# Kernel tuning notes

Hardware: AMD Instinct MI355X
Metric: run time of the kernel (lower is better)

Reference implementation:

```python
import jax, jax.numpy as jnp
import numpy as np

B, D_IN, D_OUT = 8192, 4096, 4096
IN_DIMS = (64, 64)
OUT_DIMS = (64, 64)
# tt_rank_rate=0.5 over dims [64,64,64,64] -> ranks [1,32,1024,32,1]
RANKS = (1, 32, 1024, 32, 1)


def _kaiming_uniform(key, shape):
    # matches nn.init.kaiming_uniform_(a=sqrt(5)) on a (r_prev, d, r) tensor:
    # fan_in = prod(shape[1:]) = d * r, gain = sqrt(2/(1+5)) = sqrt(1/3)
    fan_in = shape[1] * shape[2]
    bound = np.sqrt(1.0 / 3.0) * np.sqrt(3.0 / fan_in)
    return jax.random.uniform(key, shape, jnp.float32, -bound, bound)


def setup_inputs() -> dict:
    key = jax.random.key(0)
    kx, k0, k1, k2, k3, kb = jax.random.split(key, 6)
    dims = list(IN_DIMS) + list(OUT_DIMS)
    shapes = [(RANKS[i], dims[i], RANKS[i + 1]) for i in range(4)]
    x = jax.random.normal(kx, (B, D_IN), jnp.float32)
    core0 = _kaiming_uniform(k0, shapes[0])  # (1, 64, 32)
    core1 = _kaiming_uniform(k1, shapes[1])  # (32, 64, 1024)
    core2 = _kaiming_uniform(k2, shapes[2])  # (1024, 64, 32)
    core3 = _kaiming_uniform(k3, shapes[3])  # (32, 64, 1)
    bb = 1.0 / np.sqrt(D_IN)
    bias = jax.random.uniform(kb, (D_OUT,), jnp.float32, -bb, bb)
    return {"x": x, "core0": core0, "core1": core1, "core2": core2,
            "core3": core3, "bias": bias}


def reference(x, core0, core1, core2, core3, bias):
    b = x.shape[0]
    s = x.reshape(b, IN_DIMS[0], IN_DIMS[1])          # (B, 64, 64)
    # input core 0: contract first input dim (rank-in = 1 squeezed)
    s = jnp.einsum('bcd,cs->bds', s, core0[0])        # (B, 64, 32)
    # input core 1: contract second input dim and rank
    s = jnp.einsum('bcr,rcs->bs', s, core1)           # (B, 1024)
    # output core 2: expand first output dim
    s = jnp.einsum('br,rAs->bAs', s, core2)           # (B, 64, 32)
    # output core 3: expand second output dim (rank-out = 1 squeezed)
    s = jnp.einsum('bAr,rB->bAB', s, core3[..., 0])   # (B, 64, 64)
    return s.reshape(b, -1) + bias                    # (B, 4096)
```

## Files before the change

### kernel.cpp

```cpp
#include <hip/hip_runtime.h>
#include <hip/hip_bf16.h>


typedef _Float16 h4 __attribute__((ext_vector_type(4)));
typedef _Float16 h8 __attribute__((ext_vector_type(8)));
typedef float f32x4 __attribute__((ext_vector_type(4)));

#define BATCH 8192

__device__ __forceinline__ void gld_lds16(const void* g, void* l) {
  __builtin_amdgcn_global_load_lds(
      (__attribute__((address_space(1))) void*)(g),
      (__attribute__((address_space(3))) void*)(l), 16, 0, 0);
}

template <int PERM>
__global__ __launch_bounds__(256) void transpose_cast(
    const float* __restrict__ src, _Float16* __restrict__ dst, int K, int U) {
  __shared__ float t[64][65];
  const int k0 = blockIdx.x * 64, u0 = blockIdx.y * 64;
  const int tx = threadIdx.x & 63, ty = threadIdx.x >> 6;
  for (int i = ty; i < 64; i += 4) {
    const int k = k0 + i;
    const int sr = PERM ? ((k & 31) * 64 + (k >> 5)) : k;
    t[i][tx] = src[(size_t)sr * U + u0 + tx];
  }
  __syncthreads();
  for (int i = ty; i < 64; i += 4) {
    dst[(size_t)(u0 + i) * K + k0 + tx] = (_Float16)t[tx][i];
  }
}

__global__ __launch_bounds__(256) void stage2(const float* __restrict__ x,
                                              const float* __restrict__ c0,
                                              _Float16* __restrict__ s1) {
  __shared__ _Float16 xh[4 * 4096];
  __shared__ float c0l[2048];
  const int b0 = blockIdx.x * 4;
  const int tid = threadIdx.x;

  {
    const float4* xg = (const float4*)(x + (size_t)b0 * 4096);
#pragma unroll
    for (int k = 0; k < 16; ++k) {
      float4 v = xg[tid + 256 * k];
      h4 w = {(_Float16)v.x, (_Float16)v.y, (_Float16)v.z, (_Float16)v.w};
      ((h4*)xh)[tid + 256 * k] = w;
    }
    ((float4*)c0l)[tid] = ((const float4*)c0)[tid];
    ((float4*)c0l)[tid + 256] = ((const float4*)c0)[tid + 256];
  }
  __syncthreads();

  const int row = tid >> 6, t6 = tid & 63;
  const int d0 = (t6 >> 3) * 8;
  const int r0 = (t6 & 7) * 4;
  const _Float16* xrow = xh + row * 4096;

  float acc[8][4];
#pragma unroll
  for (int i = 0; i < 8; ++i)
#pragma unroll
    for (int j = 0; j < 4; ++j) acc[i][j] = 0.0f;

  for (int c = 0; c < 64; ++c) {
    h8 xv = *(const h8*)&xrow[c * 64 + d0];
    f32x4 wv = *(const f32x4*)&c0l[c * 32 + r0];
#pragma unroll
    for (int i = 0; i < 8; ++i) {
      const float xf = (float)xv[i];
#pragma unroll
      for (int j = 0; j < 4; ++j) acc[i][j] += xf * wv[j];
    }
  }

  _Float16* s1row = s1 + (size_t)(b0 + row) * 2048;
#pragma unroll
  for (int i = 0; i < 8; ++i) {
    h4 o = {(_Float16)acc[i][0], (_Float16)acc[i][1], (_Float16)acc[i][2],
            (_Float16)acc[i][3]};
    *(h4*)&s1row[(d0 + i) * 32 + r0] = o;
  }
}

template <int M, int N, int K>
__global__ __launch_bounds__(256, 3) void gemm_tn(
    const _Float16* __restrict__ A, const _Float16* __restrict__ Bt,
    _Float16* __restrict__ C) {
  __shared__ _Float16 lA[128 * 64];
  __shared__ _Float16 lB[128 * 64];
  const int bm = blockIdx.x, bn = blockIdx.y;
  const int tid = threadIdx.x;
  const int w = tid >> 6, lane = tid & 63;
  const int wm = (w >> 1) << 6, wn = (w & 1) << 6;
  const int lr = lane & 15, kh = lane >> 4;

  f32x4 acc[4][4] = {};

  const int sr = (w << 5) + (lane >> 3);
  const int sc = ((lane & 7) ^ (lane >> 3)) << 4;
  const char* gA = (const char*)(A + (size_t)(bm * 128 + sr) * K) + sc;
  const char* gB = (const char*)(Bt + (size_t)(bn * 128 + sr) * K) + sc;
  char* lAw = (char*)lA + w * 4096;
  char* lBw = (char*)lB + w * 4096;

  for (int kt = 0; kt < K / 64; ++kt) {
    __syncthreads();
    const size_t go = (size_t)kt * 128;
#pragma unroll
    for (int i = 0; i < 4; ++i) {
      gld_lds16(gA + go + (size_t)(i * 8) * (K * 2), lAw + i * 1024);
      gld_lds16(gB + go + (size_t)(i * 8) * (K * 2), lBw + i * 1024);
    }
    __syncthreads();
#pragma unroll
    for (int kk = 0; kk < 2; ++kk) {
      h8 af[4], bf[4];
#pragma unroll
      for (int m = 0; m < 4; ++m) {
        const int R = wm + m * 16 + lr;
        af[m] = *(const h8*)((const char*)lA + R * 128 +
                             ((((kk << 2) + kh) ^ (R & 7)) << 4));
      }
#pragma unroll
      for (int n = 0; n < 4; ++n) {
        const int R = wn + n * 16 + lr;
        bf[n] = *(const h8*)((const char*)lB + R * 128 +
                             ((((kk << 2) + kh) ^ (R & 7)) << 4));
      }
#pragma unroll
      for (int m = 0; m < 4; ++m)
#pragma unroll
        for (int n = 0; n < 4; ++n)
          acc[m][n] = __builtin_amdgcn_mfma_f32_16x16x32_f16(af[m], bf[n],
                                                             acc[m][n], 0, 0, 0);
    }
  }

#pragma unroll
  for (int m = 0; m < 4; ++m) {
    const int r0 = bm * 128 + wm + m * 16 + kh * 4;
#pragma unroll
    for (int n = 0; n < 4; ++n) {
      const int c0 = bn * 128 + wn + n * 16 + lr;
#pragma unroll
      for (int q = 0; q < 4; ++q)
        C[(size_t)(r0 + q) * N + c0] = (_Float16)acc[m][n][q];
    }
  }
}

__global__ __launch_bounds__(256) void stage5(const _Float16* __restrict__ s3,
                                              const float* __restrict__ c3,
                                              const float* __restrict__ bias,
                                              float* __restrict__ out) {
  __shared__ float s3t[4][2048];
  __shared__ float c3l[2048];
  const int b0 = blockIdx.x * 4;
  const int tid = threadIdx.x;
  const int row = tid >> 6, t6 = tid & 63;

  {
    const _Float16* sg = s3 + (size_t)(b0 + row) * 2048;
    const int Aj = t6 & 15, t0 = (t6 >> 4) * 8;
#pragma unroll
    for (int k = 0; k < 4; ++k) {
      const int A = Aj + 16 * k;
      h8 v = *(const h8*)&sg[A * 32 + t0];
#pragma unroll
      for (int u = 0; u < 8; ++u) s3t[row][(t0 + u) * 64 + A] = (float)v[u];
    }
    ((float4*)c3l)[tid] = ((const float4*)c3)[tid];
    ((float4*)c3l)[tid + 256] = ((const float4*)c3)[tid + 256];
  }
  __syncthreads();

  const int A0 = (t6 >> 3) * 8;
  const int B0 = (t6 & 7) * 8;

  float acc[8][8];
#pragma unroll
  for (int i = 0; i < 8; ++i)
#pragma unroll
    for (int j = 0; j < 8; ++j) acc[i][j] = 0.0f;

  for (int t = 0; t < 32; ++t) {
    f32x4 sa0 = *(const f32x4*)&s3t[row][t * 64 + A0];
    f32x4 sa1 = *(const f32x4*)&s3t[row][t * 64 + A0 + 4];
    f32x4 cb0 = *(const f32x4*)&c3l[t * 64 + B0];
    f32x4 cb1 = *(const f32x4*)&c3l[t * 64 + B0 + 4];
#pragma unroll
    for (int i = 0; i < 4; ++i) {
#pragma unroll
      for (int j = 0; j < 4; ++j) {
        acc[i][j] += sa0[i] * cb0[j];
        acc[i][j + 4] += sa0[i] * cb1[j];
        acc[i + 4][j] += sa1[i] * cb0[j];
        acc[i + 4][j + 4] += sa1[i] * cb1[j];
      }
    }
  }

  float* orow = out + (size_t)(b0 + row) * 4096;
#pragma unroll
  for (int i = 0; i < 8; ++i) {
    const int o = (A0 + i) * 64 + B0;
    f32x4 bv0 = *(const f32x4*)&bias[o];
    f32x4 bv1 = *(const f32x4*)&bias[o + 4];
    f32x4 r0, r1;
#pragma unroll
    for (int j = 0; j < 4; ++j) {
      r0[j] = acc[i][j] + bv0[j];
      r1[j] = acc[i][j + 4] + bv1[j];
    }
    *(f32x4*)&orow[o] = r0;
    *(f32x4*)&orow[o + 4] = r1;
  }
}

extern "C" void kernel_launch(void* const* d_in, const int* in_sizes, int n_in,
                              void* d_out, int out_size, void* d_ws,
                              size_t ws_size, hipStream_t stream) {
  (void)in_sizes; (void)n_in; (void)out_size; (void)ws_size;
  const float* x     = (const float*)d_in[0];
  const float* core0 = (const float*)d_in[1];
  const float* core1 = (const float*)d_in[2];
  const float* core2 = (const float*)d_in[3];
  const float* core3 = (const float*)d_in[4];
  const float* bias  = (const float*)d_in[5];
  float* out = (float*)d_out;

  char* ws = (char*)d_ws;
  _Float16* s1h = (_Float16*)ws;
  _Float16* s2h = (_Float16*)(ws + 33554432);
  _Float16* W1t = (_Float16*)(ws + 50331648);
  _Float16* W2t = (_Float16*)(ws + 54525952);

  transpose_cast<1><<<dim3(32, 16), 256, 0, stream>>>(core1, W1t, 2048, 1024);
  transpose_cast<0><<<dim3(16, 32), 256, 0, stream>>>(core2, W2t, 1024, 2048);
  stage2<<<BATCH / 4, 256, 0, stream>>>(x, core0, s1h);
  gemm_tn<BATCH, 1024, 2048><<<dim3(BATCH / 128, 1024 / 128), 256, 0, stream>>>(s1h, W1t, s2h);
  gemm_tn<BATCH, 2048, 1024><<<dim3(BATCH / 128, 2048 / 128), 256, 0, stream>>>(s2h, W2t, s1h);
  stage5<<<BATCH / 4, 256, 0, stream>>>(s1h, core3, bias, out);
}
```

Measured before the change: 175.7 us.

## Fuse core3 contraction and bias into second GEMM epilogue via MFMA

The second TT GEMM now stages its fp16 tile in LDS and runs the core3 contraction (rank 32 to 64 outputs) as extra MFMA ops. It then adds bias and writes fp32 output directly, which removes the stage5 kernel and the round-trip of the 32 MB intermediate through global memory. The two weight transpose kernels are also merged into one launch. In exchange, the core3 contraction now uses fp16 inputs instead of fp32, and the epilogue makes strided scattered stores to the output.

```diff
diff --git a/kernel.cpp b/kernel.cpp
--- a/kernel.cpp
+++ b/kernel.cpp
@@ -14,15 +14,20 @@
       (__attribute__((address_space(3))) void*)(l), 16, 0, 0);
 }
 
-template <int PERM>
-__global__ __launch_bounds__(256) void transpose_cast(
-    const float* __restrict__ src, _Float16* __restrict__ dst, int K, int U) {
+__global__ __launch_bounds__(256) void transpose_cast2(
+    const float* __restrict__ c1, _Float16* __restrict__ W1t,
+    const float* __restrict__ c2, _Float16* __restrict__ W2t) {
   __shared__ float t[64][65];
-  const int k0 = blockIdx.x * 64, u0 = blockIdx.y * 64;
+  const int which = blockIdx.z;
+  const float* src = which ? c2 : c1;
+  _Float16* dst = which ? W2t : W1t;
+  const int K = which ? 1024 : 2048, U = which ? 2048 : 1024;
+  const int k0 = (which ? blockIdx.y : blockIdx.x) * 64;
+  const int u0 = (which ? blockIdx.x : blockIdx.y) * 64;
   const int tx = threadIdx.x & 63, ty = threadIdx.x >> 6;
   for (int i = ty; i < 64; i += 4) {
     const int k = k0 + i;
-    const int sr = PERM ? ((k & 31) * 64 + (k >> 5)) : k;
+    const int sr = which ? k : ((k & 31) * 64 + (k >> 5));
     t[i][tx] = src[(size_t)sr * U + u0 + tx];
   }
   __syncthreads();
@@ -150,71 +155,112 @@
   }
 }
 
-__global__ __launch_bounds__(256) void stage5(const _Float16* __restrict__ s3,
-                                              const float* __restrict__ c3,
-                                              const float* __restrict__ bias,
-                                              float* __restrict__ out) {
-  __shared__ float s3t[4][2048];
-  __shared__ float c3l[2048];
-  const int b0 = blockIdx.x * 4;
+template <int M, int K>
+__global__ __launch_bounds__(256, 3) void gemm2_fused(
+    const _Float16* __restrict__ A, const _Float16* __restrict__ Bt,
+    const float* __restrict__ c3, const float* __restrict__ bias,
+    float* __restrict__ out) {
+  __shared__ _Float16 lds[128 * 128];
+  _Float16* lA = lds;
+  _Float16* lB = lds + 128 * 64;
+  const int bm = blockIdx.x, bn = blockIdx.y;
   const int tid = threadIdx.x;
-  const int row = tid >> 6, t6 = tid & 63;
-
-  {
-    const _Float16* sg = s3 + (size_t)(b0 + row) * 2048;
-    const int Aj = t6 & 15, t0 = (t6 >> 4) * 8;
-#pragma unroll
-    for (int k = 0; k < 4; ++k) {
-      const int A = Aj + 16 * k;
-      h8 v = *(const h8*)&sg[A * 32 + t0];
-#pragma unroll
-      for (int u = 0; u < 8; ++u) s3t[row][(t0 + u) * 64 + A] = (float)v[u];
-    }
-    ((float4*)c3l)[tid] = ((const float4*)c3)[tid];
-    ((float4*)c3l)[tid + 256] = ((const float4*)c3)[tid + 256];
-  }
-  __syncthreads();
-
-  const int A0 = (t6 >> 3) * 8;
-  const int B0 = (t6 & 7) * 8;
-
-  float acc[8][8];
-#pragma unroll
-  for (int i = 0; i < 8; ++i)
-#pragma unroll
-    for (int j = 0; j < 8; ++j) acc[i][j] = 0.0f;
-
-  for (int t = 0; t < 32; ++t) {
-    f32x4 sa0 = *(const f32x4*)&s3t[row][t * 64 + A0];
-    f32x4 sa1 = *(const f32x4*)&s3t[row][t * 64 + A0 + 4];
-    f32x4 cb0 = *(const f32x4*)&c3l[t * 64 + B0];
-    f32x4 cb1 = *(const f32x4*)&c3l[t * 64 + B0 + 4];
+  const int w = tid >> 6, lane = tid & 63;
+  const int wm = (w >> 1) << 6, wn = (w & 1) << 6;
+  const int lr = lane & 15, kh = lane >> 4;
+
+  f32x4 acc[4][4] = {};
+
+  const int sr = (w << 5) + (lane >> 3);
+  const int sc = ((lane & 7) ^ (lane >> 3)) << 4;
+  const char* gA = (const char*)(A + (size_t)(bm * 128 + sr) * K) + sc;
+  const char* gB = (const char*)(Bt + (size_t)(bn * 128 + sr) * K) + sc;
+  char* lAw = (char*)lA + w * 4096;
+  char* lBw = (char*)lB + w * 4096;
+
+  for (int kt = 0; kt < K / 64; ++kt) {
+    __syncthreads();
+    const size_t go = (size_t)kt * 128;
 #pragma unroll
     for (int i = 0; i < 4; ++i) {
-#pragma unroll
-      for (int j = 0; j < 4; ++j) {
-        acc[i][j] += sa0[i] * cb0[j];
-        acc[i][j + 4] += sa0[i] * cb1[j];
-        acc[i + 4][j] += sa1[i] * cb0[j];
-        acc[i + 4][j + 4] += sa1[i] * cb1[j];
-      }
-    }
-  }
-
-  float* orow = out + (size_t)(b0 + row) * 4096;
-#pragma unroll
-  for (int i = 0; i < 8; ++i) {
-    const int o = (A0 + i) * 64 + B0;
-    f32x4 bv0 = *(const f32x4*)&bias[o];
-    f32x4 bv1 = *(const f32x4*)&bias[o + 4];
-    f32x4 r0, r1;
-#pragma unroll
-    for (int j = 0; j < 4; ++j) {
-      r0[j] = acc[i][j] + bv0[j];
-      r1[j] = acc[i][j + 4] + bv1[j];
-    }
-    *(f32x4*)&orow[o] = r0;
-    *(f32x4*)&orow[o + 4] = r1;
+      gld_lds16(gA + go + (size_t)(i * 8) * (K * 2), lAw + i * 1024);
+      gld_lds16(gB + go + (size_t)(i * 8) * (K * 2), lBw + i * 1024);
+    }
+    __syncthreads();
+#pragma unroll
+    for (int kk = 0; kk < 2; ++kk) {
+      h8 af[4], bf[4];
+#pragma unroll
+      for (int m = 0; m < 4; ++m) {
+        const int R = wm + m * 16 + lr;
+        af[m] = *(const h8*)((const char*)lA + R * 128 +
+                             ((((kk << 2) + kh) ^ (R & 7)) << 4));
+      }
+#pragma unroll
+      for (int n = 0; n < 4; ++n) {
+        const int R = wn + n * 16 + lr;
+        bf[n] = *(const h8*)((const char*)lB + R * 128 +
+                             ((((kk << 2) + kh) ^ (R & 7)) << 4));
+      }
+#pragma unroll
+      for (int m = 0; m < 4; ++m)
+#pragma unroll
+        for (int n = 0; n < 4; ++n)
+          acc[m][n] = __builtin_amdgcn_mfma_f32_16x16x32_f16(af[m], bf[n],
+                                                             acc[m][n], 0, 0, 0);
+    }
+  }
+
+  __syncthreads();
+
+  h8 bfe[4];
+  float bb[4][4];
+#pragma unroll
+  for (int n = 0; n < 4; ++n) {
+#pragma unroll
+    for (int j = 0; j < 8; ++j)
+      bfe[n][j] = (_Float16)c3[(kh * 8 + j) * 64 + n * 16 + lr];
+#pragma unroll
+    for (int a = 0; a < 4; ++a)
+      bb[a][n] = bias[bn * 256 + a * 64 + n * 16 + lr];
+  }
+
+#pragma unroll
+  for (int m = 0; m < 4; ++m) {
+    const int Rb = wm + m * 16 + kh * 4;
+#pragma unroll
+    for (int n = 0; n < 4; ++n) {
+      const int cc = wn + n * 16 + lr;
+#pragma unroll
+      for (int q = 0; q < 4; ++q) {
+        const int R = Rb + q;
+        const int byte =
+            R * 256 + ((((cc >> 3) ^ (R & 7)) << 4) | ((cc & 7) << 1));
+        *(_Float16*)((char*)lds + byte) = (_Float16)acc[m][n][q];
+      }
+    }
+  }
+  __syncthreads();
+
+  const int wrow = w << 5;
+#pragma unroll
+  for (int mi = 0; mi < 2; ++mi) {
+    const int row = wrow + mi * 16 + lr;
+    const int orow0 = bm * 128 + wrow + mi * 16 + kh * 4;
+#pragma unroll
+    for (int a = 0; a < 4; ++a) {
+      h8 af = *(const h8*)((const char*)lds + row * 256 +
+                           ((((a << 2) + kh) ^ (row & 7)) << 4));
+#pragma unroll
+      for (int n = 0; n < 4; ++n) {
+        f32x4 d = {};
+        d = __builtin_amdgcn_mfma_f32_16x16x32_f16(af, bfe[n], d, 0, 0, 0);
+        const int ocol = bn * 256 + a * 64 + n * 16 + lr;
+#pragma unroll
+        for (int q = 0; q < 4; ++q)
+          out[(size_t)(orow0 + q) * 4096 + ocol] = d[q] + bb[a][n];
+      }
+    }
   }
 }
 
@@ -236,10 +282,8 @@
   _Float16* W1t = (_Float16*)(ws + 50331648);
   _Float16* W2t = (_Float16*)(ws + 54525952);
 
-  transpose_cast<1><<<dim3(32, 16), 256, 0, stream>>>(core1, W1t, 2048, 1024);
-  transpose_cast<0><<<dim3(16, 32), 256, 0, stream>>>(core2, W2t, 1024, 2048);
+  transpose_cast2<<<dim3(32, 16, 2), 256, 0, stream>>>(core1, W1t, core2, W2t);
   stage2<<<BATCH / 4, 256, 0, stream>>>(x, core0, s1h);
   gemm_tn<BATCH, 1024, 2048><<<dim3(BATCH / 128, 1024 / 128), 256, 0, stream>>>(s1h, W1t, s2h);
-  gemm_tn<BATCH, 2048, 1024><<<dim3(BATCH / 128, 2048 / 128), 256, 0, stream>>>(s2h, W2t, s1h);
-  stage5<<<BATCH / 4, 256, 0, stream>>>(s1h, core3, bias, out);
-}
+  gemm2_fused<BATCH, 1024><<<dim3(BATCH / 128, 2048 / 128), 256, 0, stream>>>(s2h, W2t, core3, bias, out);
+}
```

Result: faster. 150.0 us (-14.6%).
